# Kernel tuning notes

Measured on AMD Instinct MI355X. Metric: run time of the kernel, lower is better.

Reference implementation:

```python
import jax, jax.numpy as jnp
import numpy as np

GRID_SIZE = 8
SPLINE_ORDER = 3
GRID_LO, GRID_HI = -1.0, 1.0
EPS = 1e-5  # InstanceNorm2d default eps
C = 16
K = GRID_SIZE + SPLINE_ORDER  # number of B-spline basis channels per input channel


def make_grid():
    h = (GRID_HI - GRID_LO) / GRID_SIZE
    # extended knot vector, length grid_size + 2*spline_order + 1
    return jnp.arange(-SPLINE_ORDER, GRID_SIZE + SPLINE_ORDER + 1, dtype=jnp.float32) * h + GRID_LO


def bspline_bases(x, grid):
    # x: [B,C,H,W] -> bases: [B,C,H,W,K] via Cox-de Boor recursion
    xu = x[..., None]
    bases = ((xu >= grid[:-1]) & (xu < grid[1:])).astype(x.dtype)
    for k in range(1, SPLINE_ORDER + 1):
        left = grid[:-(k + 1)]
        right = grid[k:-1]
        delta = jnp.where(right == left, jnp.ones_like(right), right - left)
        bases = ((xu - left) / delta) * bases[..., :-1] + \
                ((grid[k + 1:] - xu) / (grid[k + 1:] - grid[1:-k])) * bases[..., 1:]
    return bases


def conv2d(x, w):
    # NCHW conv, stride 1, padding 1 (kernel 3x3), bias=False as in KANConv2DLayer
    return jax.lax.conv_general_dilated(
        x, w, window_strides=(1, 1), padding=[(1, 1), (1, 1)],
        dimension_numbers=('NCHW', 'OIHW', 'NCHW'))


def instance_norm(x):
    # nn.InstanceNorm2d(affine=False): normalize over H,W per (N,C)
    m = jnp.mean(x, axis=(2, 3), keepdims=True)
    v = jnp.var(x, axis=(2, 3), keepdims=True)
    return (x - m) * jax.lax.rsqrt(v + EPS)


def prelu(x, a):
    return jnp.where(x >= 0, x, a * x)


def kan_conv_layer(x, base_w, spline_w, prelu_a, grid):
    base_out = conv2d(jax.nn.silu(x), base_w)
    b = bspline_bases(x, grid)                      # [B,C,H,W,K]
    B, Cx, H, W, Kx = b.shape
    b = jnp.moveaxis(b, -1, 2).reshape(B, Cx * Kx, H, W)
    spline_out = conv2d(b, spline_w)
    return prelu(instance_norm(base_out + spline_out), prelu_a)


def setup_inputs() -> dict:
    key = jax.random.key(0)
    ks = jax.random.split(key, 5)
    s = 0.05
    return {
        'x': jax.random.normal(ks[0], (4, C, 512, 512), jnp.float32),
        'base_w1': jax.random.normal(ks[1], (C, C, 3, 3), jnp.float32) * s,
        'spline_w1': jax.random.normal(ks[2], (C, C * K, 3, 3), jnp.float32) * s,
        'prelu_a1': jnp.float32(0.25),
        'base_w2': jax.random.normal(ks[3], (C, C, 3, 3), jnp.float32) * s,
        'spline_w2': jax.random.normal(ks[4], (C, C * K, 3, 3), jnp.float32) * s,
        'prelu_a2': jnp.float32(0.25),
    }


def reference(x, base_w1, spline_w1, prelu_a1, base_w2, spline_w2, prelu_a2):
    grid = make_grid()
    y = kan_conv_layer(x, base_w1, spline_w1, prelu_a1, grid)
    y = kan_conv_layer(y, base_w2, spline_w2, prelu_a2, grid)
    return jax.nn.sigmoid(y)
```

## Files before the change

kernel.cpp:

```cpp
#include <hip/hip_runtime.h>
#include <cstddef>
#include <cstdint>

#define HW    512
#define CCH   16
#define HTILE 18
#define NPIX  324
#define NSLOT 12

typedef _Float16 f16x8 __attribute__((ext_vector_type(8)));
typedef float    f32x4 __attribute__((ext_vector_type(4)));

__device__ __forceinline__ float h2f(ushort u) {
    _Float16 h = __builtin_bit_cast(_Float16, u);
    return (float)h;
}
__device__ __forceinline__ ushort f2h(float f) {
    _Float16 h = (_Float16)f;
    return __builtin_bit_cast(ushort, h);
}
__device__ __forceinline__ uint pack2h(float a, float b) {
    return (uint)f2h(a) | ((uint)f2h(b) << 16);
}

__device__ __forceinline__ void derived12(float x, uint* u) {
    float si = x / (1.0f + __expf(-x));
    float t  = fmaf(x, 4.0f, 7.0f);
    t = fminf(fmaxf(t, -1.0f), 15.0f);
    float ft = floorf(t);
    int   ci = (int)ft;
    float uu = t - ft;
    float um = 1.0f - uu;
    float u2 = uu * uu, m2 = um * um;
    float u3 = u2 * uu, m3 = m2 * um;
    const float c16 = 0.16666667f, c23 = 0.66666667f;
    float w0 = u3 * c16;
    float w3 = m3 * c16;
    float w2 = fmaf(0.5f, u3, c23 - u2);
    float w1 = fmaf(0.5f, m3, c23 - m2);
    uint64_t P = (uint64_t)f2h(w3)
               | ((uint64_t)f2h(w2) << 16)
               | ((uint64_t)f2h(w1) << 32)
               | ((uint64_t)f2h(w0) << 48);
    int s = 16 * ci - 48;
    int d = s >> 6;
    int e = s & 63;
    uint64_t Q = P << e;
    uint64_t R = (P >> (63 - e)) >> 1;
    uint64_t O0 = (d == 0) ? Q : (d == -1) ? R : 0ull;
    uint64_t O1 = (d == 1) ? Q : (d ==  0) ? R : 0ull;
    uint64_t O2 = (d == 2) ? Q : (d ==  1) ? R : 0ull;
    O2 = (O2 & 0x0000ffffffffffffull) | ((uint64_t)f2h(si) << 48);
    u[0] = (uint)O0; u[1] = (uint)(O0 >> 32);
    u[2] = (uint)O1; u[3] = (uint)(O1 >> 32);
    u[4] = (uint)O2; u[5] = (uint)(O2 >> 32);
}

__global__ void __launch_bounds__(64) prep_w(
    const float* __restrict__ bw1, const float* __restrict__ sw1,
    const float* __restrict__ bw2, const float* __restrict__ sw2,
    uint4* __restrict__ wtab1, uint4* __restrict__ wtab2)
{
    const int s    = blockIdx.x;
    const int lane = threadIdx.x;
    const float* bw; const float* sw; uint4* wt;
    if (blockIdx.y == 0) { bw = bw1; sw = sw1; wt = wtab1; }
    else                 { bw = bw2; sw = sw2; wt = wtab2; }
    const int co = lane & 15, q = lane >> 4;
    const int chunk = s / 27, sl = s - chunk * 27;
    uint u[4];
#pragma unroll
    for (int jj = 0; jj < 4; ++jj) {
        float w[2];
#pragma unroll
        for (int h = 0; h < 2; ++h) {
            int j   = jj * 2 + h;
            int kl  = 32 * sl + 8 * q + j;
            int tap = kl / 96;
            int r   = kl - tap * 96;
            int ci  = r / 12;
            int kv  = r - ci * 12;
            int cin = chunk * 8 + ci;
            w[h] = (kv == 11) ? bw[(co * 16 + cin) * 9 + tap]
                              : sw[(co * 176 + cin * 11 + kv) * 9 + tap];
        }
        u[jj] = pack2h(w[0], w[1]);
    }
    wt[s * 64 + lane] = make_uint4(u[0], u[1], u[2], u[3]);
}

template<bool IN_H, bool OUT_H>
__global__ __launch_bounds__(256, 2) void conv_mfma(
    const void* __restrict__ in_v,
    const uint4* __restrict__ wtab,
    void* __restrict__ out_v)
{
    __shared__ uint4 dt16[NSLOT * NPIX];

    const int tid  = threadIdx.x;
    const int lane = tid & 63;
    const int wv   = tid >> 6;
    const int m    = lane & 15;
    const int q    = lane >> 4;
    const int bx0  = blockIdx.x * 16;
    const int by0  = blockIdx.y * 16;
    const int b    = blockIdx.z;

    const float*  inf = (const float*)in_v;
    const ushort* inh = (const ushort*)in_v;

    f32x4 acc[4];
#pragma unroll
    for (int t = 0; t < 4; ++t) acc[t] = f32x4{0.f, 0.f, 0.f, 0.f};

#pragma unroll 1
    for (int chunk = 0; chunk < 2; ++chunk) {
        __syncthreads();

        {
            float v0[6], v1[6];
            uint  bofs[6];
            bool  live[6];
#pragma unroll
            for (int k = 0; k < 6; ++k) {
                int it  = tid + k * 256;
                bool lv = (it < NPIX * 4);
                int cp  = it / NPIX;
                int pix = it - cp * NPIX;
                int py  = pix / 18;
                int px  = pix - py * 18;
                int gy  = by0 + py - 1;
                int gx  = bx0 + px - 1;
                bool ok = lv && ((unsigned)gy < (unsigned)HW)
                             && ((unsigned)gx < (unsigned)HW);
                live[k] = lv;
                bofs[k] = (uint)(cp * 3 * NPIX + pix);
                float a = -1.0e9f, c = -1.0e9f;
                if (ok) {
                    size_t base = ((size_t)(b * CCH + chunk * 8 + cp * 2) << 18)
                                + ((size_t)gy << 9) + gx;
                    if (IN_H) { a = h2f(inh[base]); c = h2f(inh[base + (1u << 18)]); }
                    else      { a = inf[base];      c = inf[base + (1u << 18)]; }
                }
                v0[k] = a; v1[k] = c;
            }
#pragma unroll
            for (int k = 0; k < 6; ++k) {
                if (live[k]) {
                    uint uA[6], uB[6];
                    derived12(v0[k], uA);
                    derived12(v1[k], uB);
                    uint bo = bofs[k];
                    dt16[bo]            = make_uint4(uA[0], uA[1], uA[2], uA[3]);
                    dt16[bo + NPIX]     = make_uint4(uA[4], uA[5], uB[0], uB[1]);
                    dt16[bo + 2 * NPIX] = make_uint4(uB[2], uB[3], uB[4], uB[5]);
                }
            }
        }
        __syncthreads();

        uint4 wf[27];
#pragma unroll
        for (int s = 0; s < 27; ++s) wf[s] = wtab[(chunk * 27 + s) * 64 + lane];

        const uint rbase = (uint)(q * NPIX + wv * 72 + m);
#pragma unroll
        for (int s = 0; s < 27; ++s) {
            const int tap = s / 3;
            const int tdy = tap / 3, tdx = tap - tdy * 3;
            const int j   = s - tap * 3;
#pragma unroll
            for (int t = 0; t < 4; ++t) {
                uint off = rbase + (uint)(j * (4 * NPIX) + (t + tdy) * HTILE + tdx);
                f16x8 a = *reinterpret_cast<const f16x8*>(&dt16[off]);
                acc[t] = __builtin_amdgcn_mfma_f32_16x16x32_f16(
                    __builtin_bit_cast(f16x8, wf[s]), a, acc[t], 0, 0, 0);
            }
        }
    }

#pragma unroll
    for (int t = 0; t < 4; ++t) {
        int oy = by0 + wv * 4 + t;
#pragma unroll
        for (int r = 0; r < 4; ++r) {
            int co = q * 4 + r;
            size_t idx = ((size_t)(b * CCH + co) << 18) + ((size_t)oy << 9) + (bx0 + m);
            if (OUT_H) ((ushort*)out_v)[idx] = f2h(acc[t][r]);
            else       ((float*)out_v)[idx]  = acc[t][r];
        }
    }
}

__global__ void __launch_bounds__(256) reduce_partial_h(
    const ushort* __restrict__ zh, float* __restrict__ part)
{
    const int bc = blockIdx.y;
    const uint* p = (const uint*)(zh + ((size_t)bc << 18) + ((size_t)blockIdx.x << 12));
    float s = 0.0f, qq = 0.0f;
    for (int i = threadIdx.x; i < 2048; i += 256) {
        uint u = p[i];
        float a = h2f((ushort)(u & 0xffffu));
        float c = h2f((ushort)(u >> 16));
        s += a + c;
        qq = fmaf(a, a, qq);
        qq = fmaf(c, c, qq);
    }
#pragma unroll
    for (int off = 32; off > 0; off >>= 1) {
        s  += __shfl_down(s, off);
        qq += __shfl_down(qq, off);
    }
    __shared__ float ls[4], lq[4];
    const int wid = threadIdx.x >> 6;
    if ((threadIdx.x & 63) == 0) { ls[wid] = s; lq[wid] = qq; }
    __syncthreads();
    if (threadIdx.x == 0) {
        part[((size_t)bc * 64 + blockIdx.x) * 2]     = ls[0] + ls[1] + ls[2] + ls[3];
        part[((size_t)bc * 64 + blockIdx.x) * 2 + 1] = lq[0] + lq[1] + lq[2] + lq[3];
    }
}

__global__ void __launch_bounds__(256) reduce_partial(
    const float* __restrict__ z, float* __restrict__ part)
{
    const int bc = blockIdx.y;
    const float* p = z + ((size_t)bc << 18) + ((size_t)blockIdx.x << 12);
    float s = 0.0f, qq = 0.0f;
    for (int i = threadIdx.x; i < 4096; i += 256) {
        float v = p[i];
        s += v;
        qq = fmaf(v, v, qq);
    }
#pragma unroll
    for (int off = 32; off > 0; off >>= 1) {
        s  += __shfl_down(s, off);
        qq += __shfl_down(qq, off);
    }
    __shared__ float ls[4], lq[4];
    const int wid = threadIdx.x >> 6;
    if ((threadIdx.x & 63) == 0) { ls[wid] = s; lq[wid] = qq; }
    __syncthreads();
    if (threadIdx.x == 0) {
        part[((size_t)bc * 64 + blockIdx.x) * 2]     = ls[0] + ls[1] + ls[2] + ls[3];
        part[((size_t)bc * 64 + blockIdx.x) * 2 + 1] = lq[0] + lq[1] + lq[2] + lq[3];
    }
}

__global__ void __launch_bounds__(256) reduce_final(
    const float* __restrict__ part, float* __restrict__ stats)
{
    const int tid = threadIdx.x;
    const int bc  = tid >> 2;
    const int j   = tid & 3;
    float s = 0.0f, qq = 0.0f;
    for (int i = j; i < 64; i += 4) {
        s  += part[((size_t)bc * 64 + i) * 2];
        qq += part[((size_t)bc * 64 + i) * 2 + 1];
    }
    s  += __shfl_down(s, 1);  s  += __shfl_down(s, 2);
    qq += __shfl_down(qq, 1); qq += __shfl_down(qq, 2);
    if (j == 0) {
        const float inv = 1.0f / 262144.0f;
        float mval = s * inv;
        float var  = qq * inv - mval * mval;
        stats[bc * 2]     = mval;
        stats[bc * 2 + 1] = rsqrtf(var + 1e-5f);
    }
}

__global__ void __launch_bounds__(256) norm_prelu_h(
    ushort* __restrict__ y, const float* __restrict__ stats,
    const float* __restrict__ a_ptr)
{
    const float a = *a_ptr;
    const int i2 = blockIdx.x * 256 + threadIdx.x;
    const int bc = i2 >> 16;
    const float mm = stats[bc * 2];
    const float rr = stats[bc * 2 + 1];
    uint2* py = (uint2*)y;
    uint2 v = py[i2];
    float f0 = h2f((ushort)(v.x & 0xffffu)), f1 = h2f((ushort)(v.x >> 16));
    float f2 = h2f((ushort)(v.y & 0xffffu)), f3 = h2f((ushort)(v.y >> 16));
    f0 = (f0 - mm) * rr; f0 = (f0 >= 0.f) ? f0 : a * f0;
    f1 = (f1 - mm) * rr; f1 = (f1 >= 0.f) ? f1 : a * f1;
    f2 = (f2 - mm) * rr; f2 = (f2 >= 0.f) ? f2 : a * f2;
    f3 = (f3 - mm) * rr; f3 = (f3 >= 0.f) ? f3 : a * f3;
    v.x = pack2h(f0, f1);
    v.y = pack2h(f2, f3);
    py[i2] = v;
}

__global__ void __launch_bounds__(256) final_sigmoid(
    float* __restrict__ out, const float* __restrict__ stats,
    const float* __restrict__ a_ptr)
{
    const float a = *a_ptr;
    const int i4 = blockIdx.x * 256 + threadIdx.x;
    const int bc = i4 >> 16;
    const float mm = stats[bc * 2];
    const float rr = stats[bc * 2 + 1];
    float4 v = reinterpret_cast<float4*>(out)[i4];
    float t;
    t = (v.x - mm) * rr; t = (t >= 0.f) ? t : a * t; v.x = 1.0f / (1.0f + __expf(-t));
    t = (v.y - mm) * rr; t = (t >= 0.f) ? t : a * t; v.y = 1.0f / (1.0f + __expf(-t));
    t = (v.z - mm) * rr; t = (t >= 0.f) ? t : a * t; v.z = 1.0f / (1.0f + __expf(-t));
    t = (v.w - mm) * rr; t = (t >= 0.f) ? t : a * t; v.w = 1.0f / (1.0f + __expf(-t));
    reinterpret_cast<float4*>(out)[i4] = v;
}

extern "C" void kernel_launch(void* const* d_in, const int* in_sizes, int n_in,
                              void* d_out, int out_size, void* d_ws, size_t ws_size,
                              hipStream_t stream)
{
    const float* x        = (const float*)d_in[0];
    const float* base_w1  = (const float*)d_in[1];
    const float* spline_w1= (const float*)d_in[2];
    const float* prelu_a1 = (const float*)d_in[3];
    const float* base_w2  = (const float*)d_in[4];
    const float* spline_w2= (const float*)d_in[5];
    const float* prelu_a2 = (const float*)d_in[6];
    float* out_f = (float*)d_out;
    char*  wsb   = (char*)d_ws;

    ushort* z1h    = (ushort*)wsb;
    uint4*  wtab1  = (uint4*)(wsb + 33554432);
    uint4*  wtab2  = (uint4*)(wsb + 33609728);
    float*  part   = (float*)(wsb + 33665024);
    float*  stats1 = (float*)(wsb + 33697792);
    float*  stats2 = (float*)(wsb + 33698304);

    dim3 cgrid(HW / 16, HW / 16, 4);
    dim3 cblk(256);
    dim3 rgrid(64, 64);

    prep_w<<<dim3(54, 2), 64, 0, stream>>>(base_w1, spline_w1, base_w2, spline_w2,
                                           wtab1, wtab2);

    conv_mfma<false, true><<<cgrid, cblk, 0, stream>>>(x, wtab1, z1h);
    reduce_partial_h<<<rgrid, cblk, 0, stream>>>(z1h, part);
    reduce_final<<<1, 256, 0, stream>>>(part, stats1);
    norm_prelu_h<<<16384, cblk, 0, stream>>>(z1h, stats1, prelu_a1);

    conv_mfma<true, false><<<cgrid, cblk, 0, stream>>>(z1h, wtab2, out_f);
    reduce_partial<<<rgrid, cblk, 0, stream>>>(out_f, part);
    reduce_final<<<1, 256, 0, stream>>>(part, stats2);

    final_sigmoid<<<16384, cblk, 0, stream>>>(out_f, stats2, prelu_a2);
}
```

Measured before the change: 415.7 us.

## Fuse instance-norm statistics and PReLU into conv kernels, reuse LDS rows across taps

The conv kernel now accumulates per-channel sum and sum-of-squares from its fp32 accumulators and adds them to a small per-(batch,channel) buffer with atomics. This removes the separate partial-reduction passes over the intermediate tensors. The second conv applies the first layer's normalization and PReLU while staging its input, which removes the standalone norm_prelu pass that read and wrote the fp16 intermediate. The MFMA loop is reordered so each loaded B-row is reused across the three vertical taps, and the weight loads are issued before the LDS staging. In exchange the statistics now come from fp32 accumulators rather than the fp16-rounded stores, summation order is non-deterministic because of the atomics, and the conv uses more registers.

```diff
diff --git a/kernel.cpp b/kernel.cpp
--- a/kernel.cpp
+++ b/kernel.cpp
@@ -59,13 +59,21 @@
 __global__ void __launch_bounds__(64) prep_w(
     const float* __restrict__ bw1, const float* __restrict__ sw1,
     const float* __restrict__ bw2, const float* __restrict__ sw2,
-    uint4* __restrict__ wtab1, uint4* __restrict__ wtab2)
+    uint4* __restrict__ wtab1, uint4* __restrict__ wtab2,
+    float* __restrict__ part1, float* __restrict__ part2)
 {
     const int s    = blockIdx.x;
     const int lane = threadIdx.x;
     const float* bw; const float* sw; uint4* wt;
     if (blockIdx.y == 0) { bw = bw1; sw = sw1; wt = wtab1; }
     else                 { bw = bw2; sw = sw2; wt = wtab2; }
+
+    if (s == 0) {
+        float* p = (blockIdx.y == 0) ? part1 : part2;
+        p[lane] = 0.0f;
+        p[64 + lane] = 0.0f;
+    }
+
     const int co = lane & 15, q = lane >> 4;
     const int chunk = s / 27, sl = s - chunk * 27;
     uint u[4];
@@ -89,13 +97,17 @@
     wt[s * 64 + lane] = make_uint4(u[0], u[1], u[2], u[3]);
 }
 
-template<bool IN_H, bool OUT_H>
+template<bool IN_H, bool OUT_H, bool NORM_IN>
 __global__ __launch_bounds__(256, 2) void conv_mfma(
     const void* __restrict__ in_v,
     const uint4* __restrict__ wtab,
-    void* __restrict__ out_v)
+    void* __restrict__ out_v,
+    const float* __restrict__ stats_in,
+    const float* __restrict__ a_in,
+    float* __restrict__ part_out)
 {
     __shared__ uint4 dt16[NSLOT * NPIX];
+    __shared__ float sn[32];
 
     const int tid  = threadIdx.x;
     const int lane = tid & 63;
@@ -109,6 +121,12 @@
     const float*  inf = (const float*)in_v;
     const ushort* inh = (const ushort*)in_v;
 
+    float pa = 0.0f;
+    if (NORM_IN) {
+        pa = *a_in;
+        if (tid < 32) sn[tid] = stats_in[b * 32 + tid];
+    }
+
     f32x4 acc[4];
 #pragma unroll
     for (int t = 0; t < 4; ++t) acc[t] = f32x4{0.f, 0.f, 0.f, 0.f};
@@ -117,64 +135,81 @@
     for (int chunk = 0; chunk < 2; ++chunk) {
         __syncthreads();
 
-        {
-            float v0[6], v1[6];
-            uint  bofs[6];
-            bool  live[6];
-#pragma unroll
-            for (int k = 0; k < 6; ++k) {
-                int it  = tid + k * 256;
-                bool lv = (it < NPIX * 4);
-                int cp  = it / NPIX;
-                int pix = it - cp * NPIX;
-                int py  = pix / 18;
-                int px  = pix - py * 18;
-                int gy  = by0 + py - 1;
-                int gx  = bx0 + px - 1;
-                bool ok = lv && ((unsigned)gy < (unsigned)HW)
-                             && ((unsigned)gx < (unsigned)HW);
-                live[k] = lv;
-                bofs[k] = (uint)(cp * 3 * NPIX + pix);
-                float a = -1.0e9f, c = -1.0e9f;
-                if (ok) {
-                    size_t base = ((size_t)(b * CCH + chunk * 8 + cp * 2) << 18)
-                                + ((size_t)gy << 9) + gx;
-                    if (IN_H) { a = h2f(inh[base]); c = h2f(inh[base + (1u << 18)]); }
-                    else      { a = inf[base];      c = inf[base + (1u << 18)]; }
+        float v0[6], v1[6];
+        uint  bofs[6], cps[6];
+        bool  live[6];
+#pragma unroll
+        for (int k = 0; k < 6; ++k) {
+            int it  = tid + k * 256;
+            bool lv = (it < NPIX * 4);
+            int cp  = it / NPIX;
+            int pix = it - cp * NPIX;
+            int py  = pix / 18;
+            int px  = pix - py * 18;
+            int gy  = by0 + py - 1;
+            int gx  = bx0 + px - 1;
+            bool ok = lv && ((unsigned)gy < (unsigned)HW)
+                         && ((unsigned)gx < (unsigned)HW);
+            live[k] = lv;
+            cps[k]  = (uint)cp;
+            bofs[k] = (uint)(cp * 3 * NPIX + pix);
+            float a = -1.0e9f, c = -1.0e9f;
+            if (ok) {
+                size_t base = ((size_t)(b * CCH + chunk * 8 + cp * 2) << 18)
+                            + ((size_t)gy << 9) + gx;
+                if (IN_H) { a = h2f(inh[base]); c = h2f(inh[base + (1u << 18)]); }
+                else      { a = inf[base];      c = inf[base + (1u << 18)]; }
+            }
+            v0[k] = a; v1[k] = c;
+        }
+
+        uint4 wf[27];
+#pragma unroll
+        for (int s = 0; s < 27; ++s) wf[s] = wtab[(chunk * 27 + s) * 64 + lane];
+
+#pragma unroll
+        for (int k = 0; k < 6; ++k) {
+            if (live[k]) {
+                float a0 = v0[k], c0 = v1[k];
+                if (NORM_IN) {
+                    int ci2 = (chunk * 8 + (int)cps[k] * 2) * 2;
+                    a0 = (a0 - sn[ci2])     * sn[ci2 + 1];
+                    a0 = (a0 >= 0.f) ? a0 : pa * a0;
+                    c0 = (c0 - sn[ci2 + 2]) * sn[ci2 + 3];
+                    c0 = (c0 >= 0.f) ? c0 : pa * c0;
                 }
-                v0[k] = a; v1[k] = c;
+                uint uA[6], uB[6];
+                derived12(a0, uA);
+                derived12(c0, uB);
+                uint bo = bofs[k];
+                dt16[bo]            = make_uint4(uA[0], uA[1], uA[2], uA[3]);
+                dt16[bo + NPIX]     = make_uint4(uA[4], uA[5], uB[0], uB[1]);
+                dt16[bo + 2 * NPIX] = make_uint4(uB[2], uB[3], uB[4], uB[5]);
             }
-#pragma unroll
-            for (int k = 0; k < 6; ++k) {
-                if (live[k]) {
-                    uint uA[6], uB[6];
-                    derived12(v0[k], uA);
-                    derived12(v1[k], uB);
-                    uint bo = bofs[k];
-                    dt16[bo]            = make_uint4(uA[0], uA[1], uA[2], uA[3]);
-                    dt16[bo + NPIX]     = make_uint4(uA[4], uA[5], uB[0], uB[1]);
-                    dt16[bo + 2 * NPIX] = make_uint4(uB[2], uB[3], uB[4], uB[5]);
+        }
+        __syncthreads();
+
+        const uint pixbase = (uint)(wv * 72 + m);
+#pragma unroll
+        for (int j = 0; j < 3; ++j) {
+            const uint slotoff = (uint)((j * 4 + q) * NPIX) + pixbase;
+#pragma unroll
+            for (int tdx = 0; tdx < 3; ++tdx) {
+                f16x8 brow[6];
+#pragma unroll
+                for (int r6 = 0; r6 < 6; ++r6)
+                    brow[r6] = *reinterpret_cast<const f16x8*>(
+                        &dt16[slotoff + (uint)(r6 * HTILE + tdx)]);
+#pragma unroll
+                for (int tdy = 0; tdy < 3; ++tdy) {
+                    const int s = (tdy * 3 + tdx) * 3 + j;
+#pragma unroll
+                    for (int t = 0; t < 4; ++t) {
+                        acc[t] = __builtin_amdgcn_mfma_f32_16x16x32_f16(
+                            __builtin_bit_cast(f16x8, wf[s]), brow[t + tdy],
+                            acc[t], 0, 0, 0);
+                    }
                 }
-            }
-        }
-        __syncthreads();
-
-        uint4 wf[27];
-#pragma unroll
-        for (int s = 0; s < 27; ++s) wf[s] = wtab[(chunk * 27 + s) * 64 + lane];
-
-        const uint rbase = (uint)(q * NPIX + wv * 72 + m);
-#pragma unroll
-        for (int s = 0; s < 27; ++s) {
-            const int tap = s / 3;
-            const int tdy = tap / 3, tdx = tap - tdy * 3;
-            const int j   = s - tap * 3;
-#pragma unroll
-            for (int t = 0; t < 4; ++t) {
-                uint off = rbase + (uint)(j * (4 * NPIX) + (t + tdy) * HTILE + tdx);
-                f16x8 a = *reinterpret_cast<const f16x8*>(&dt16[off]);
-                acc[t] = __builtin_amdgcn_mfma_f32_16x16x32_f16(
-                    __builtin_bit_cast(f16x8, wf[s]), a, acc[t], 0, 0, 0);
             }
         }
     }
@@ -190,105 +225,52 @@
             else       ((float*)out_v)[idx]  = acc[t][r];
         }
     }
-}
-
-__global__ void __launch_bounds__(256) reduce_partial_h(
-    const ushort* __restrict__ zh, float* __restrict__ part)
-{
-    const int bc = blockIdx.y;
-    const uint* p = (const uint*)(zh + ((size_t)bc << 18) + ((size_t)blockIdx.x << 12));
-    float s = 0.0f, qq = 0.0f;
-    for (int i = threadIdx.x; i < 2048; i += 256) {
-        uint u = p[i];
-        float a = h2f((ushort)(u & 0xffffu));
-        float c = h2f((ushort)(u >> 16));
-        s += a + c;
-        qq = fmaf(a, a, qq);
-        qq = fmaf(c, c, qq);
-    }
-#pragma unroll
-    for (int off = 32; off > 0; off >>= 1) {
-        s  += __shfl_down(s, off);
-        qq += __shfl_down(qq, off);
-    }
-    __shared__ float ls[4], lq[4];
-    const int wid = threadIdx.x >> 6;
-    if ((threadIdx.x & 63) == 0) { ls[wid] = s; lq[wid] = qq; }
+
+    float s4[4], q4[4];
+#pragma unroll
+    for (int r = 0; r < 4; ++r) {
+        s4[r] = acc[0][r] + acc[1][r] + acc[2][r] + acc[3][r];
+        q4[r] = fmaf(acc[0][r], acc[0][r],
+                fmaf(acc[1][r], acc[1][r],
+                fmaf(acc[2][r], acc[2][r], acc[3][r] * acc[3][r])));
+    }
+#pragma unroll
+    for (int off = 8; off > 0; off >>= 1) {
+#pragma unroll
+        for (int r = 0; r < 4; ++r) {
+            s4[r] += __shfl_xor(s4[r], off);
+            q4[r] += __shfl_xor(q4[r], off);
+        }
+    }
     __syncthreads();
-    if (threadIdx.x == 0) {
-        part[((size_t)bc * 64 + blockIdx.x) * 2]     = ls[0] + ls[1] + ls[2] + ls[3];
-        part[((size_t)bc * 64 + blockIdx.x) * 2 + 1] = lq[0] + lq[1] + lq[2] + lq[3];
-    }
-}
-
-__global__ void __launch_bounds__(256) reduce_partial(
-    const float* __restrict__ z, float* __restrict__ part)
-{
-    const int bc = blockIdx.y;
-    const float* p = z + ((size_t)bc << 18) + ((size_t)blockIdx.x << 12);
-    float s = 0.0f, qq = 0.0f;
-    for (int i = threadIdx.x; i < 4096; i += 256) {
-        float v = p[i];
-        s += v;
-        qq = fmaf(v, v, qq);
-    }
-#pragma unroll
-    for (int off = 32; off > 0; off >>= 1) {
-        s  += __shfl_down(s, off);
-        qq += __shfl_down(qq, off);
-    }
-    __shared__ float ls[4], lq[4];
-    const int wid = threadIdx.x >> 6;
-    if ((threadIdx.x & 63) == 0) { ls[wid] = s; lq[wid] = qq; }
+    float* scr = (float*)dt16;
+    if (m == 0) {
+#pragma unroll
+        for (int r = 0; r < 4; ++r) {
+            scr[(wv * 16 + q * 4 + r) * 2 + 0] = s4[r];
+            scr[(wv * 16 + q * 4 + r) * 2 + 1] = q4[r];
+        }
+    }
     __syncthreads();
-    if (threadIdx.x == 0) {
-        part[((size_t)bc * 64 + blockIdx.x) * 2]     = ls[0] + ls[1] + ls[2] + ls[3];
-        part[((size_t)bc * 64 + blockIdx.x) * 2 + 1] = lq[0] + lq[1] + lq[2] + lq[3];
-    }
-}
-
-__global__ void __launch_bounds__(256) reduce_final(
+    if (tid < 32) {
+        int co = tid >> 1, which = tid & 1;
+        float v = scr[(0 * 16 + co) * 2 + which] + scr[(1 * 16 + co) * 2 + which]
+                + scr[(2 * 16 + co) * 2 + which] + scr[(3 * 16 + co) * 2 + which];
+        atomicAdd(&part_out[(size_t)(b * CCH + co) * 2 + which], v);
+    }
+}
+
+__global__ void __launch_bounds__(64) reduce_final(
     const float* __restrict__ part, float* __restrict__ stats)
 {
-    const int tid = threadIdx.x;
-    const int bc  = tid >> 2;
-    const int j   = tid & 3;
-    float s = 0.0f, qq = 0.0f;
-    for (int i = j; i < 64; i += 4) {
-        s  += part[((size_t)bc * 64 + i) * 2];
-        qq += part[((size_t)bc * 64 + i) * 2 + 1];
-    }
-    s  += __shfl_down(s, 1);  s  += __shfl_down(s, 2);
-    qq += __shfl_down(qq, 1); qq += __shfl_down(qq, 2);
-    if (j == 0) {
-        const float inv = 1.0f / 262144.0f;
-        float mval = s * inv;
-        float var  = qq * inv - mval * mval;
-        stats[bc * 2]     = mval;
-        stats[bc * 2 + 1] = rsqrtf(var + 1e-5f);
-    }
-}
-
-__global__ void __launch_bounds__(256) norm_prelu_h(
-    ushort* __restrict__ y, const float* __restrict__ stats,
-    const float* __restrict__ a_ptr)
-{
-    const float a = *a_ptr;
-    const int i2 = blockIdx.x * 256 + threadIdx.x;
-    const int bc = i2 >> 16;
-    const float mm = stats[bc * 2];
-    const float rr = stats[bc * 2 + 1];
-    uint2* py = (uint2*)y;
-    uint2 v = py[i2];
-    float f0 = h2f((ushort)(v.x & 0xffffu)), f1 = h2f((ushort)(v.x >> 16));
-    float f2 = h2f((ushort)(v.y & 0xffffu)), f3 = h2f((ushort)(v.y >> 16));
-    f0 = (f0 - mm) * rr; f0 = (f0 >= 0.f) ? f0 : a * f0;
-    f1 = (f1 - mm) * rr; f1 = (f1 >= 0.f) ? f1 : a * f1;
-    f2 = (f2 - mm) * rr; f2 = (f2 >= 0.f) ? f2 : a * f2;
-    f3 = (f3 - mm) * rr; f3 = (f3 >= 0.f) ? f3 : a * f3;
-    v.x = pack2h(f0, f1);
-    v.y = pack2h(f2, f3);
-    py[i2] = v;
+    const int bc = threadIdx.x;
+    const float inv = 1.0f / 262144.0f;
+    float s  = part[bc * 2];
+    float qq = part[bc * 2 + 1];
+    float mval = s * inv;
+    float var  = qq * inv - mval * mval;
+    stats[bc * 2]     = mval;
+    stats[bc * 2 + 1] = rsqrtf(var + 1e-5f);
 }
 
 __global__ void __launch_bounds__(256) final_sigmoid(
@@ -326,25 +308,24 @@
     ushort* z1h    = (ushort*)wsb;
     uint4*  wtab1  = (uint4*)(wsb + 33554432);
     uint4*  wtab2  = (uint4*)(wsb + 33609728);
-    float*  part   = (float*)(wsb + 33665024);
-    float*  stats1 = (float*)(wsb + 33697792);
-    float*  stats2 = (float*)(wsb + 33698304);
+    float*  part1  = (float*)(wsb + 33665024);
+    float*  part2  = (float*)(wsb + 33665536);
+    float*  stats1 = (float*)(wsb + 33666048);
+    float*  stats2 = (float*)(wsb + 33666560);
 
     dim3 cgrid(HW / 16, HW / 16, 4);
     dim3 cblk(256);
-    dim3 rgrid(64, 64);
 
     prep_w<<<dim3(54, 2), 64, 0, stream>>>(base_w1, spline_w1, base_w2, spline_w2,
-                                           wtab1, wtab2);
-
-    conv_mfma<false, true><<<cgrid, cblk, 0, stream>>>(x, wtab1, z1h);
-    reduce_partial_h<<<rgrid, cblk, 0, stream>>>(z1h, part);
-    reduce_final<<<1, 256, 0, stream>>>(part, stats1);
-    norm_prelu_h<<<16384, cblk, 0, stream>>>(z1h, stats1, prelu_a1);
-
-    conv_mfma<true, false><<<cgrid, cblk, 0, stream>>>(z1h, wtab2, out_f);
-    reduce_partial<<<rgrid, cblk, 0, stream>>>(out_f, part);
-    reduce_final<<<1, 256, 0, stream>>>(part, stats2);
+                                           wtab1, wtab2, part1, part2);
+
+    conv_mfma<false, true, false><<<cgrid, cblk, 0, stream>>>(
+        x, wtab1, z1h, nullptr, nullptr, part1);
+    reduce_final<<<1, 64, 0, stream>>>(part1, stats1);
+
+    conv_mfma<true, false, true><<<cgrid, cblk, 0, stream>>>(
+        z1h, wtab2, out_f, stats1, prelu_a1, part2);
+    reduce_final<<<1, 64, 0, stream>>>(part2, stats2);
 
     final_sigmoid<<<16384, cblk, 0, stream>>>(out_f, stats2, prelu_a2);
 }
```

Result: faster. 356.0 us (-14.4%).
